# Optimization experiments

Hardware: AMD Instinct MI355X
Metric: run time of the kernel (lower is better)

## Reference

```python
import jax, jax.numpy as jnp
import numpy as np

B, S, K_IN = 8, 2048, 512
D_MODEL, N_INPUT, N_PROCESS = 1024, 4096, 2048
K = 256


def setup_inputs() -> dict:
    key = jax.random.key(0)
    k1, k2, k3, k4 = jax.random.split(key, 4)
    return {
        "selected_activations": jax.random.normal(k1, (B, S, K_IN), dtype=jnp.float32),
        "selected_indices": jax.random.randint(k2, (B, K_IN), 0, N_INPUT, dtype=jnp.int64),
        "k": K,
        "combination_weights": jax.random.normal(k3, (N_PROCESS, N_INPUT), dtype=jnp.float32),
        "output_projections": jax.random.normal(k4, (N_PROCESS, D_MODEL), dtype=jnp.float32),
    }


def reference(selected_activations, selected_indices, k, combination_weights, output_projections):
    # Gather per-batch combination weights: [n_process, B, k_in] -> [B, n_process, k_in]
    sel_w = jnp.take(combination_weights, selected_indices, axis=1)  # [P, B, k_in]
    sel_w = jnp.transpose(sel_w, (1, 0, 2))                          # [B, P, k_in]
    # Batched matmul + exact GELU (torch F.gelu default is erf-based)
    process_act = jax.nn.gelu(
        jnp.einsum("bsk,bpk->bsp", selected_activations, sel_w), approximate=False
    )  # [B, S, P]
    # Top-k gating over mean activation across sequence
    process_scores = process_act.mean(axis=1)                        # [B, P]
    _, proc_idx = jax.lax.top_k(process_scores, k)                   # [B, k]
    # Gather selected process activations along last dim
    sel_proc_act = jnp.take_along_axis(process_act, proc_idx[:, None, :], axis=2)  # [B, S, k]
    # Gather output projections per batch: [B, k, d_model]
    sel_proj = output_projections[proc_idx]                          # [B, k, D]
    return jnp.einsum("bsk,bkd->bsd", sel_proc_act, sel_proj)        # [B, S, D]
```

## Files before the change

### kernel.cpp

```cpp
#include <hip/hip_runtime.h>
#include <hip/hip_bf16.h>
#include <math.h>

#define B_    8
#define S_    2048
#define KIN_  512
#define NIN_  4096
#define P_    2048
#define D_    1024
#define KSEL_ 256

typedef __attribute__((ext_vector_type(8))) short short8;
typedef __attribute__((ext_vector_type(4))) float f32x4;

__device__ __forceinline__ unsigned short f2bf(float f) {
    unsigned u = __float_as_uint(f);
    unsigned r = (u + 0x7fffu + ((u >> 16) & 1u)) >> 16;
    return (unsigned short)r;
}
__device__ __forceinline__ float bf2f(unsigned short h) {
    return __uint_as_float(((unsigned)h) << 16);
}
__device__ __forceinline__ float gelu_exact(float x) {
    return 0.5f * x * (1.0f + erff(x * 0.70710678118654752f));
}
__device__ __forceinline__ void gl2lds16(const void* g, void* l) {
    __builtin_amdgcn_global_load_lds(
        (const __attribute__((address_space(1))) unsigned int*)g,
        (__attribute__((address_space(3))) unsigned int*)l, 16, 0, 0);
}

__global__ __launch_bounds__(256) void prep_kernel(
        const float* __restrict__ A, const float* __restrict__ W,
        const int* __restrict__ idx,
        unsigned short* __restrict__ Ahi, unsigned short* __restrict__ Alo,
        unsigned short* __restrict__ Ghi, unsigned short* __restrict__ Glo) {
    int id = blockIdx.x;
    if (id < 8192) {
        size_t i = (size_t)id * 256 + threadIdx.x;
        float4 v = reinterpret_cast<const float4*>(A)[i];
        ushort4 hi, lo;
        hi.x = f2bf(v.x); lo.x = f2bf(v.x - bf2f(hi.x));
        hi.y = f2bf(v.y); lo.y = f2bf(v.y - bf2f(hi.y));
        hi.z = f2bf(v.z); lo.z = f2bf(v.z - bf2f(hi.z));
        hi.w = f2bf(v.w); lo.w = f2bf(v.w - bf2f(hi.w));
        reinterpret_cast<ushort4*>(Ahi)[i] = hi;
        reinterpret_cast<ushort4*>(Alo)[i] = lo;
    } else {
        int bp = id - 8192;
        int b  = bp >> 11;
        const int* ib = idx + (size_t)b * KIN_;
        const float* wrow = W + (size_t)(bp & 2047) * NIN_;
        size_t o = (size_t)bp * KIN_;
        for (int j = threadIdx.x; j < KIN_; j += 256) {
            float v = wrow[ib[j]];
            unsigned short h = f2bf(v);
            Ghi[o + j] = h;
            Glo[o + j] = f2bf(v - bf2f(h));
        }
    }
}

template <bool STORE_C>
__global__ __launch_bounds__(256) void gemm1_score(
        const unsigned short* __restrict__ Ahi, const unsigned short* __restrict__ Alo,
        const unsigned short* __restrict__ Ghi, const unsigned short* __restrict__ Glo,
        float* __restrict__ scores, unsigned short* __restrict__ C) {
    __shared__ __align__(16) unsigned short lds[32768];

    int d    = blockIdx.x;
    int xcd  = d & 7;
    int slot = d >> 3;
    int c    = (slot >> 4) * 8 + xcd;
    int j    = slot & 15;
    int b    = c >> 4;
    int rc   = c & 15;
    int p0   = ((rc & 3) * 4 + (j & 3)) * 128;
    int s0   = ((rc >> 2) * 4 + (j >> 2)) * 128;

    const int t  = threadIdx.x;
    const int w = t >> 6, l = t & 63;
    const int wm = w & 1, wn = w >> 1;
    const int lr = l & 15, quad = l >> 4;

    const int srow = t >> 2;
    const int koff = (t & 3) * 8;
    const size_t baseA = ((size_t)(b * S_ + s0)) * KIN_;
    const size_t baseG = ((size_t)(b * P_ + p0)) * KIN_;
    const unsigned short* pA0 = Ahi + baseA + (size_t)srow * KIN_ + koff;
    const unsigned short* pA1 = pA0 + (size_t)64 * KIN_;
    const unsigned short* pL0 = Alo + baseA + (size_t)srow * KIN_ + koff;
    const unsigned short* pL1 = pL0 + (size_t)64 * KIN_;
    const unsigned short* pG0 = Ghi + baseG + (size_t)srow * KIN_ + koff;
    const unsigned short* pG1 = pG0 + (size_t)64 * KIN_;
    const unsigned short* pH0 = Glo + baseG + (size_t)srow * KIN_ + koff;
    const unsigned short* pH1 = pH0 + (size_t)64 * KIN_;
    char* lb = (char*)lds + w * 1024;

    int ra[4], rg[4];
#pragma unroll
    for (int i = 0; i < 4; i++) {
        ra[i] = (wm * 64 + i * 16 + lr) * 32 + quad * 8;
        rg[i] = (wn * 64 + i * 16 + lr) * 32 + quad * 8;
    }

    f32x4 acc[4][4];
#pragma unroll
    for (int i = 0; i < 4; i++)
#pragma unroll
        for (int jj = 0; jj < 4; jj++) acc[i][jj] = (f32x4){0.f, 0.f, 0.f, 0.f};

    auto issue = [&](int k0, int buf) {
        char* dst = lb + buf * 32768;
        gl2lds16(pA0 + k0, dst + 0);
        gl2lds16(pA1 + k0, dst + 4096);
        gl2lds16(pL0 + k0, dst + 8192);
        gl2lds16(pL1 + k0, dst + 12288);
        gl2lds16(pG0 + k0, dst + 16384);
        gl2lds16(pG1 + k0, dst + 20480);
        gl2lds16(pH0 + k0, dst + 24576);
        gl2lds16(pH1 + k0, dst + 28672);
    };

    issue(0, 0);
    for (int it = 0; it < KIN_ / 32; ++it) {
        if (it + 1 < KIN_ / 32) {
            issue((it + 1) * 32, (it + 1) & 1);
            asm volatile("s_waitcnt vmcnt(8)\n\ts_barrier" ::: "memory");
        } else {
            asm volatile("s_waitcnt vmcnt(0)\n\ts_barrier" ::: "memory");
        }
        const unsigned short* Lb = lds + (it & 1) * 16384;

        short8 gh[4], gl8[4];
#pragma unroll
        for (int i = 0; i < 4; i++) {
            gh[i]  = *(const short8*)(Lb + 8192 + rg[i]);
            gl8[i] = *(const short8*)(Lb + 12288 + rg[i]);
        }
#pragma unroll
        for (int mt = 0; mt < 4; mt++) {
            short8 ah = *(const short8*)(Lb + ra[mt]);
            short8 al = *(const short8*)(Lb + 4096 + ra[mt]);
#pragma unroll
            for (int nt = 0; nt < 4; nt++) {
                acc[mt][nt] = __builtin_amdgcn_mfma_f32_16x16x32_bf16(ah, gh[nt],  acc[mt][nt], 0, 0, 0);
                acc[mt][nt] = __builtin_amdgcn_mfma_f32_16x16x32_bf16(ah, gl8[nt], acc[mt][nt], 0, 0, 0);
                acc[mt][nt] = __builtin_amdgcn_mfma_f32_16x16x32_bf16(al, gh[nt],  acc[mt][nt], 0, 0, 0);
            }
        }
        asm volatile("s_barrier" ::: "memory");
    }

    float colsum[4] = {0.f, 0.f, 0.f, 0.f};
#pragma unroll
    for (int mt = 0; mt < 4; mt++)
#pragma unroll
        for (int nt = 0; nt < 4; nt++)
#pragma unroll
            for (int r = 0; r < 4; r++) {
                float g = gelu_exact(acc[mt][nt][r]);
                colsum[nt] += g;
                acc[mt][nt][r] = g;
            }
#pragma unroll
    for (int nt = 0; nt < 4; nt++) {
        colsum[nt] += __shfl_xor(colsum[nt], 16);
        colsum[nt] += __shfl_xor(colsum[nt], 32);
    }
    if (quad == 0) {
#pragma unroll
        for (int nt = 0; nt < 4; nt++)
            atomicAdd(&scores[b * P_ + p0 + wn * 64 + nt * 16 + lr], colsum[nt]);
    }

    if (STORE_C) {
#pragma unroll
        for (int mt = 0; mt < 4; mt++)
#pragma unroll
            for (int nt = 0; nt < 4; nt++)
#pragma unroll
                for (int r = 0; r < 4; r++) {
                    int row = wm * 64 + mt * 16 + quad * 4 + r;
                    int col = wn * 64 + nt * 16 + lr;
                    lds[row * 128 + col] = f2bf(acc[mt][nt][r]);
                }
        __syncthreads();
        for (int i = t; i < 2048; i += 256) {
            int row = i >> 4, ch = i & 15;
            uint4 v = *(const uint4*)(lds + row * 128 + ch * 8);
            *(uint4*)(C + ((size_t)(b * S_ + s0 + row)) * P_ + p0 + ch * 8) = v;
        }
    }
}

__global__ __launch_bounds__(1024) void topk_kernel(const float* __restrict__ scores,
                                                    int* __restrict__ pidx) {
    __shared__ float v[2048];
    __shared__ int   ix[2048];
    int b = blockIdx.x;
    int t = threadIdx.x;
    for (int i = t; i < 2048; i += 1024) { v[i] = scores[b * 2048 + i]; ix[i] = i; }
    __syncthreads();
    for (int k = 2; k <= 2048; k <<= 1) {
        for (int j = k >> 1; j > 0; j >>= 1) {
            for (int i = t; i < 2048; i += 1024) {
                int o = i ^ j;
                if (o > i) {
                    bool desc = ((i & k) == 0);
                    float va = v[i], vb = v[o];
                    int ia = ix[i], ib = ix[o];
                    bool b_first = (vb > va) || (vb == va && ib < ia);
                    if (desc == b_first) { v[i] = vb; v[o] = va; ix[i] = ib; ix[o] = ia; }
                }
            }
            __syncthreads();
        }
    }
    if (t < KSEL_) pidx[b * KSEL_ + t] = ix[t];
}

__global__ __launch_bounds__(256) void gathers_kernel(
        const unsigned short* __restrict__ C, const float* __restrict__ proj,
        const int* __restrict__ pidx,
        unsigned short* __restrict__ selact, unsigned short* __restrict__ PselT) {
    __shared__ int pj[256];
    __shared__ unsigned short tile[64][65];
    int id = blockIdx.x, t = threadIdx.x;
    if (id < 2048) {
        int b = id >> 8;
        pj[t] = pidx[b * KSEL_ + t];
        __syncthreads();
        size_t r0 = (size_t)b * S_ + (id & 255) * 8;
#pragma unroll
        for (int r = 0; r < 8; ++r) {
            size_t row = r0 + r;
            selact[row * KSEL_ + t] = C[row * P_ + pj[t]];
        }
    } else {
        int g = id - 2048;
        int d0 = (g & 15) * 64, k0 = ((g >> 4) & 3) * 64, b = g >> 6;
        int tr = t >> 6;
        int tc = t & 63;
#pragma unroll
        for (int r = 0; r < 16; r++) {
            int kk = r * 4 + tr;
            int prow = pidx[b * KSEL_ + k0 + kk];
            tile[kk][tc] = f2bf(proj[(size_t)prow * D_ + d0 + tc]);
        }
        __syncthreads();
#pragma unroll
        for (int r = 0; r < 16; r++) {
            int dd = r * 4 + tr;
            PselT[((size_t)(b * D_ + d0 + dd)) * KSEL_ + k0 + tc] = tile[tc][dd];
        }
    }
}

__global__ __launch_bounds__(256) void gemm1b_selact(
        const unsigned short* __restrict__ Ahi, const unsigned short* __restrict__ Alo,
        const unsigned short* __restrict__ Ghi, const unsigned short* __restrict__ Glo,
        const int* __restrict__ pidx, unsigned short* __restrict__ selact) {
    __shared__ __align__(16) unsigned short lds[16384];

    const int t  = threadIdx.x;
    const int b  = blockIdx.z;
    const int s0 = blockIdx.y * 128;
    const int n0 = blockIdx.x * 128;
    const int w = t >> 6, l = t & 63;
    const int wm = w & 1, wn = w >> 1;
    const int lr = l & 15, quad = l >> 4;

    const int srow = t >> 2;
    const int koff = (t & 3) * 8;
    const size_t baseA = ((size_t)(b * S_ + s0)) * KIN_;
    const size_t offA0 = baseA + (size_t)srow * KIN_ + koff;
    const size_t offA1 = offA0 + (size_t)64 * KIN_;
    const int prow0 = pidx[b * KSEL_ + n0 + srow];
    const int prow1 = pidx[b * KSEL_ + n0 + 64 + srow];
    const size_t offG0 = ((size_t)(b * P_ + prow0)) * KIN_ + koff;
    const size_t offG1 = ((size_t)(b * P_ + prow1)) * KIN_ + koff;
    char* lb = (char*)lds + w * 1024;

    int ra[4], rg[4];
#pragma unroll
    for (int i = 0; i < 4; i++) {
        ra[i] = (wm * 64 + i * 16 + lr) * 32 + quad * 8;
        rg[i] = (wn * 64 + i * 16 + lr) * 32 + quad * 8;
    }

    f32x4 acc[4][4];
#pragma unroll
    for (int i = 0; i < 4; i++)
#pragma unroll
        for (int j = 0; j < 4; j++) acc[i][j] = (f32x4){0.f, 0.f, 0.f, 0.f};

    for (int k0 = 0; k0 < KIN_; k0 += 32) {
        gl2lds16(Ahi + offA0 + k0, lb + 0);
        gl2lds16(Ahi + offA1 + k0, lb + 4096);
        gl2lds16(Alo + offA0 + k0, lb + 8192);
        gl2lds16(Alo + offA1 + k0, lb + 12288);
        gl2lds16(Ghi + offG0 + k0, lb + 16384);
        gl2lds16(Ghi + offG1 + k0, lb + 20480);
        gl2lds16(Glo + offG0 + k0, lb + 24576);
        gl2lds16(Glo + offG1 + k0, lb + 28672);
        __syncthreads();

        short8 ah[4], al8[4], gh[4], gl8[4];
#pragma unroll
        for (int i = 0; i < 4; i++) {
            ah[i]  = *(const short8*)(lds + ra[i]);
            al8[i] = *(const short8*)(lds + 4096 + ra[i]);
            gh[i]  = *(const short8*)(lds + 8192 + rg[i]);
            gl8[i] = *(const short8*)(lds + 12288 + rg[i]);
        }
#pragma unroll
        for (int mt = 0; mt < 4; mt++)
#pragma unroll
            for (int nt = 0; nt < 4; nt++) {
                acc[mt][nt] = __builtin_amdgcn_mfma_f32_16x16x32_bf16(ah[mt],  gh[nt],  acc[mt][nt], 0, 0, 0);
                acc[mt][nt] = __builtin_amdgcn_mfma_f32_16x16x32_bf16(ah[mt],  gl8[nt], acc[mt][nt], 0, 0, 0);
                acc[mt][nt] = __builtin_amdgcn_mfma_f32_16x16x32_bf16(al8[mt], gh[nt],  acc[mt][nt], 0, 0, 0);
            }
        __syncthreads();
    }

#pragma unroll
    for (int mt = 0; mt < 4; mt++)
#pragma unroll
        for (int nt = 0; nt < 4; nt++)
#pragma unroll
            for (int r = 0; r < 4; r++) {
                int row = wm * 64 + mt * 16 + quad * 4 + r;
                int col = wn * 64 + nt * 16 + lr;
                lds[row * 128 + col] = f2bf(gelu_exact(acc[mt][nt][r]));
            }
    __syncthreads();
    for (int i = t; i < 2048; i += 256) {
        int row = i >> 4, ch = i & 15;
        uint4 v = *(const uint4*)(lds + row * 128 + ch * 8);
        *(uint4*)(selact + ((size_t)(b * S_ + s0 + row)) * KSEL_ + n0 + ch * 8) = v;
    }
}

__global__ __launch_bounds__(256) void gemm2_mfma(
        const unsigned short* __restrict__ selact,
        const unsigned short* __restrict__ PselT,
        float* __restrict__ out) {
    __shared__ __align__(16) unsigned short lds[16384];

    const int t  = threadIdx.x;
    const int b  = blockIdx.z;
    const int s0 = blockIdx.y * 128;
    const int d0 = blockIdx.x * 128;
    const int w = t >> 6, l = t & 63;
    const int wm = w & 1, wn = w >> 1;
    const int lr = l & 15, quad = l >> 4;

    const int srow = t >> 2;
    const int koff = (t & 3) * 8;
    const unsigned short* pA0 = selact + ((size_t)(b * S_ + s0 + srow)) * KSEL_ + koff;
    const unsigned short* pA1 = pA0 + (size_t)64 * KSEL_;
    const unsigned short* pB0 = PselT + ((size_t)(b * D_ + d0 + srow)) * KSEL_ + koff;
    const unsigned short* pB1 = pB0 + (size_t)64 * KSEL_;
    char* lb = (char*)lds + w * 1024;

    int ra[4], rg[4];
#pragma unroll
    for (int i = 0; i < 4; i++) {
        ra[i] = (wm * 64 + i * 16 + lr) * 32 + quad * 8;
        rg[i] = (wn * 64 + i * 16 + lr) * 32 + quad * 8;
    }

    f32x4 acc[4][4];
#pragma unroll
    for (int i = 0; i < 4; i++)
#pragma unroll
        for (int j = 0; j < 4; j++) acc[i][j] = (f32x4){0.f, 0.f, 0.f, 0.f};

    auto issue = [&](int k0, int buf) {
        char* dst = lb + buf * 16384;
        gl2lds16(pA0 + k0, dst + 0);
        gl2lds16(pA1 + k0, dst + 4096);
        gl2lds16(pB0 + k0, dst + 8192);
        gl2lds16(pB1 + k0, dst + 12288);
    };

    issue(0, 0);
    for (int it = 0; it < KSEL_ / 32; ++it) {
        if (it + 1 < KSEL_ / 32) {
            issue((it + 1) * 32, (it + 1) & 1);
            asm volatile("s_waitcnt vmcnt(4)\n\ts_barrier" ::: "memory");
        } else {
            asm volatile("s_waitcnt vmcnt(0)\n\ts_barrier" ::: "memory");
        }
        const unsigned short* Lb = lds + (it & 1) * 8192;

        short8 af[4], bf[4];
#pragma unroll
        for (int i = 0; i < 4; i++) {
            af[i] = *(const short8*)(Lb + ra[i]);
            bf[i] = *(const short8*)(Lb + 4096 + rg[i]);
        }
#pragma unroll
        for (int mt = 0; mt < 4; mt++)
#pragma unroll
            for (int nt = 0; nt < 4; nt++)
                acc[mt][nt] = __builtin_amdgcn_mfma_f32_16x16x32_bf16(af[mt], bf[nt], acc[mt][nt], 0, 0, 0);
        asm volatile("s_barrier" ::: "memory");
    }

#pragma unroll
    for (int mt = 0; mt < 4; mt++)
#pragma unroll
        for (int nt = 0; nt < 4; nt++)
#pragma unroll
            for (int r = 0; r < 4; r++)
                out[((size_t)(b * S_ + s0 + wm * 64 + mt * 16 + quad * 4 + r)) * D_
                    + d0 + wn * 64 + nt * 16 + lr] = acc[mt][nt][r];
}

extern "C" void kernel_launch(void* const* d_in, const int* in_sizes, int n_in,
                              void* d_out, int out_size, void* d_ws, size_t ws_size,
                              hipStream_t stream) {
    (void)in_sizes; (void)n_in; (void)out_size;
    const float* act  = (const float*)d_in[0];
    const int*   idx  = (const int*)d_in[1];
    const float* W    = (const float*)d_in[3];
    const float* proj = (const float*)d_in[4];
    float*       out  = (float*)d_out;

    char* ws = (char*)d_ws;
    unsigned short* Ahi    = (unsigned short*)(ws + 0);
    unsigned short* Alo    = (unsigned short*)(ws + 16777216);
    unsigned short* Ghi    = (unsigned short*)(ws + 33554432);
    unsigned short* Glo    = (unsigned short*)(ws + 50331648);
    float*          scores = (float*)(ws + 67108864);
    int*            pidx   = (int*)(ws + 67174400);
    unsigned short* selact = (unsigned short*)(ws + 67182592);
    unsigned short* PselT  = (unsigned short*)(ws + 75571200);
    unsigned short* Cbf    = (unsigned short*)(ws + 79765504);
    const bool big = ws_size >= 146874368ull;

    hipMemsetAsync(scores, 0, B_ * P_ * sizeof(float), stream);

    prep_kernel<<<dim3(8192 + B_ * P_), 256, 0, stream>>>(act, W, idx, Ahi, Alo, Ghi, Glo);

    if (big) {
        gemm1_score<true><<<dim3(2048), 256, 0, stream>>>(Ahi, Alo, Ghi, Glo, scores, Cbf);
        topk_kernel<<<dim3(B_), 1024, 0, stream>>>(scores, pidx);
        gathers_kernel<<<dim3(2048 + 512), 256, 0, stream>>>(Cbf, proj, pidx, selact, PselT);
    } else {
        gemm1_score<false><<<dim3(2048), 256, 0, stream>>>(Ahi, Alo, Ghi, Glo, scores, nullptr);
        topk_kernel<<<dim3(B_), 1024, 0, stream>>>(scores, pidx);
        gemm1b_selact<<<dim3(KSEL_ / 128, S_ / 128, B_), 256, 0, stream>>>(
            Ahi, Alo, Ghi, Glo, pidx, selact);
        gathers_kernel<<<dim3(2048 + 512), 256, 0, stream>>>(Cbf, proj, pidx, selact, PselT);
    }
    gemm2_mfma<<<dim3(D_ / 128, S_ / 128, B_), 256, 0, stream>>>(selact, PselT, out);
}
```

Measured before the change: 403.3 us.

## Pre-swizzle A-lo into MFMA fragment layout, load directly to registers, XOR-swizzle LDS

The prep kernel now writes the low bf16 half of the activations in a fragment-major layout, so each lane can load its MFMA operand straight from global memory into registers. This removes the A-lo tiles from LDS staging, shrinking shared memory per block to allow three blocks per CU. LDS reads and writes in all GEMMs use an XOR swizzle on the k-chunk to reduce bank conflicts. The non-big path also stops launching the idle selact-gather blocks. The direct global loads add register pressure and rely on the cache for latency hiding.

```diff
diff --git a/kernel.cpp b/kernel.cpp
--- a/kernel.cpp
+++ b/kernel.cpp
@@ -36,23 +36,35 @@
         unsigned short* __restrict__ Ahi, unsigned short* __restrict__ Alo,
         unsigned short* __restrict__ Ghi, unsigned short* __restrict__ Glo) {
     int id = blockIdx.x;
-    if (id < 8192) {
-        size_t i = (size_t)id * 256 + threadIdx.x;
-        float4 v = reinterpret_cast<const float4*>(A)[i];
-        ushort4 hi, lo;
-        hi.x = f2bf(v.x); lo.x = f2bf(v.x - bf2f(hi.x));
-        hi.y = f2bf(v.y); lo.y = f2bf(v.y - bf2f(hi.y));
-        hi.z = f2bf(v.z); lo.z = f2bf(v.z - bf2f(hi.z));
-        hi.w = f2bf(v.w); lo.w = f2bf(v.w - bf2f(hi.w));
-        reinterpret_cast<ushort4*>(Ahi)[i] = hi;
-        reinterpret_cast<ushort4*>(Alo)[i] = lo;
+    int t  = threadIdx.x;
+    if (id < 1024) {
+        int b = id >> 7, rb = id & 127;
+        int l = t & 63, wv = t >> 6;
+        int lr = l & 15, quad = l >> 4;
+        const float* src = A + ((size_t)(b * S_ + rb * 16 + lr)) * KIN_ + quad * 8;
+        unsigned short* dh = Ahi + ((size_t)(b * S_ + rb * 16 + lr)) * KIN_ + quad * 8;
+        unsigned short* dl = Alo + (size_t)(b * 16) * 65536 + (size_t)rb * 512 + (size_t)l * 8;
+        for (int kb = wv; kb < 16; kb += 4) {
+            float4 v0 = *(const float4*)(src + kb * 32);
+            float4 v1 = *(const float4*)(src + kb * 32 + 4);
+            float vv[8] = {v0.x, v0.y, v0.z, v0.w, v1.x, v1.y, v1.z, v1.w};
+            short8 h8, l8;
+#pragma unroll
+            for (int jj = 0; jj < 8; jj++) {
+                unsigned short h = f2bf(vv[jj]);
+                h8[jj] = (short)h;
+                l8[jj] = (short)f2bf(vv[jj] - bf2f(h));
+            }
+            *(short8*)(dh + kb * 32) = h8;
+            *(short8*)(dl + (size_t)kb * 65536) = l8;
+        }
     } else {
-        int bp = id - 8192;
+        int bp = id - 1024;
         int b  = bp >> 11;
         const int* ib = idx + (size_t)b * KIN_;
         const float* wrow = W + (size_t)(bp & 2047) * NIN_;
         size_t o = (size_t)bp * KIN_;
-        for (int j = threadIdx.x; j < KIN_; j += 256) {
+        for (int j = t; j < KIN_; j += 256) {
             float v = wrow[ib[j]];
             unsigned short h = f2bf(v);
             Ghi[o + j] = h;
@@ -62,11 +74,11 @@
 }
 
 template <bool STORE_C>
-__global__ __launch_bounds__(256) void gemm1_score(
+__global__ __launch_bounds__(256, 3) void gemm1_score(
         const unsigned short* __restrict__ Ahi, const unsigned short* __restrict__ Alo,
         const unsigned short* __restrict__ Ghi, const unsigned short* __restrict__ Glo,
         float* __restrict__ scores, unsigned short* __restrict__ C) {
-    __shared__ __align__(16) unsigned short lds[32768];
+    __shared__ __align__(16) unsigned short lds[24576];
 
     int d    = blockIdx.x;
     int xcd  = d & 7;
@@ -84,24 +96,26 @@
     const int lr = l & 15, quad = l >> 4;
 
     const int srow = t >> 2;
-    const int koff = (t & 3) * 8;
+    const int koff = ((t & 3) ^ ((t >> 3) & 3)) * 8;
     const size_t baseA = ((size_t)(b * S_ + s0)) * KIN_;
     const size_t baseG = ((size_t)(b * P_ + p0)) * KIN_;
     const unsigned short* pA0 = Ahi + baseA + (size_t)srow * KIN_ + koff;
     const unsigned short* pA1 = pA0 + (size_t)64 * KIN_;
-    const unsigned short* pL0 = Alo + baseA + (size_t)srow * KIN_ + koff;
-    const unsigned short* pL1 = pL0 + (size_t)64 * KIN_;
     const unsigned short* pG0 = Ghi + baseG + (size_t)srow * KIN_ + koff;
     const unsigned short* pG1 = pG0 + (size_t)64 * KIN_;
     const unsigned short* pH0 = Glo + baseG + (size_t)srow * KIN_ + koff;
     const unsigned short* pH1 = pH0 + (size_t)64 * KIN_;
+    const unsigned short* alB = Alo + (size_t)(b * 16) * 65536
+                              + (size_t)((s0 >> 4) + wm * 4) * 512 + (size_t)l * 8;
     char* lb = (char*)lds + w * 1024;
 
     int ra[4], rg[4];
 #pragma unroll
     for (int i = 0; i < 4; i++) {
-        ra[i] = (wm * 64 + i * 16 + lr) * 32 + quad * 8;
-        rg[i] = (wn * 64 + i * 16 + lr) * 32 + quad * 8;
+        int rowa = wm * 64 + i * 16 + lr;
+        int rowg = wn * 64 + i * 16 + lr;
+        ra[i] = rowa * 32 + (quad ^ ((rowa >> 1) & 3)) * 8;
+        rg[i] = rowg * 32 + (quad ^ ((rowg >> 1) & 3)) * 8;
     }
 
     f32x4 acc[4][4];
@@ -111,42 +125,43 @@
         for (int jj = 0; jj < 4; jj++) acc[i][jj] = (f32x4){0.f, 0.f, 0.f, 0.f};
 
     auto issue = [&](int k0, int buf) {
-        char* dst = lb + buf * 32768;
+        char* dst = lb + buf * 24576;
         gl2lds16(pA0 + k0, dst + 0);
         gl2lds16(pA1 + k0, dst + 4096);
-        gl2lds16(pL0 + k0, dst + 8192);
-        gl2lds16(pL1 + k0, dst + 12288);
-        gl2lds16(pG0 + k0, dst + 16384);
-        gl2lds16(pG1 + k0, dst + 20480);
-        gl2lds16(pH0 + k0, dst + 24576);
-        gl2lds16(pH1 + k0, dst + 28672);
+        gl2lds16(pG0 + k0, dst + 8192);
+        gl2lds16(pG1 + k0, dst + 12288);
+        gl2lds16(pH0 + k0, dst + 16384);
+        gl2lds16(pH1 + k0, dst + 20480);
     };
 
     issue(0, 0);
     for (int it = 0; it < KIN_ / 32; ++it) {
+        short8 alc[4];
+#pragma unroll
+        for (int mt = 0; mt < 4; mt++)
+            alc[mt] = *(const short8*)(alB + (size_t)it * 65536 + mt * 512);
         if (it + 1 < KIN_ / 32) {
             issue((it + 1) * 32, (it + 1) & 1);
-            asm volatile("s_waitcnt vmcnt(8)\n\ts_barrier" ::: "memory");
+            asm volatile("s_waitcnt vmcnt(10)\n\ts_barrier" ::: "memory");
         } else {
             asm volatile("s_waitcnt vmcnt(0)\n\ts_barrier" ::: "memory");
         }
-        const unsigned short* Lb = lds + (it & 1) * 16384;
+        const unsigned short* Lb = lds + (it & 1) * 12288;
 
         short8 gh[4], gl8[4];
 #pragma unroll
         for (int i = 0; i < 4; i++) {
-            gh[i]  = *(const short8*)(Lb + 8192 + rg[i]);
-            gl8[i] = *(const short8*)(Lb + 12288 + rg[i]);
+            gh[i]  = *(const short8*)(Lb + 4096 + rg[i]);
+            gl8[i] = *(const short8*)(Lb + 8192 + rg[i]);
         }
 #pragma unroll
         for (int mt = 0; mt < 4; mt++) {
             short8 ah = *(const short8*)(Lb + ra[mt]);
-            short8 al = *(const short8*)(Lb + 4096 + ra[mt]);
 #pragma unroll
             for (int nt = 0; nt < 4; nt++) {
-                acc[mt][nt] = __builtin_amdgcn_mfma_f32_16x16x32_bf16(ah, gh[nt],  acc[mt][nt], 0, 0, 0);
-                acc[mt][nt] = __builtin_amdgcn_mfma_f32_16x16x32_bf16(ah, gl8[nt], acc[mt][nt], 0, 0, 0);
-                acc[mt][nt] = __builtin_amdgcn_mfma_f32_16x16x32_bf16(al, gh[nt],  acc[mt][nt], 0, 0, 0);
+                acc[mt][nt] = __builtin_amdgcn_mfma_f32_16x16x32_bf16(ah,      gh[nt],  acc[mt][nt], 0, 0, 0);
+                acc[mt][nt] = __builtin_amdgcn_mfma_f32_16x16x32_bf16(ah,      gl8[nt], acc[mt][nt], 0, 0, 0);
+                acc[mt][nt] = __builtin_amdgcn_mfma_f32_16x16x32_bf16(alc[mt], gh[nt],  acc[mt][nt], 0, 0, 0);
             }
         }
         asm volatile("s_barrier" ::: "memory");
@@ -223,10 +238,11 @@
 __global__ __launch_bounds__(256) void gathers_kernel(
         const unsigned short* __restrict__ C, const float* __restrict__ proj,
         const int* __restrict__ pidx,
-        unsigned short* __restrict__ selact, unsigned short* __restrict__ PselT) {
+        unsigned short* __restrict__ selact, unsigned short* __restrict__ PselT,
+        int base) {
     __shared__ int pj[256];
     __shared__ unsigned short tile[64][65];
-    int id = blockIdx.x, t = threadIdx.x;
+    int id = blockIdx.x + base, t = threadIdx.x;
     if (id < 2048) {
         int b = id >> 8;
         pj[t] = pidx[b * KSEL_ + t];
@@ -272,7 +288,7 @@
     const int lr = l & 15, quad = l >> 4;
 
     const int srow = t >> 2;
-    const int koff = (t & 3) * 8;
+    const int koff = ((t & 3) ^ ((t >> 3) & 3)) * 8;
     const size_t baseA = ((size_t)(b * S_ + s0)) * KIN_;
     const size_t offA0 = baseA + (size_t)srow * KIN_ + koff;
     const size_t offA1 = offA0 + (size_t)64 * KIN_;
@@ -280,48 +296,54 @@
     const int prow1 = pidx[b * KSEL_ + n0 + 64 + srow];
     const size_t offG0 = ((size_t)(b * P_ + prow0)) * KIN_ + koff;
     const size_t offG1 = ((size_t)(b * P_ + prow1)) * KIN_ + koff;
+    const unsigned short* alB = Alo + (size_t)(b * 16) * 65536
+                              + (size_t)((s0 >> 4) + wm * 4) * 512 + (size_t)l * 8;
     char* lb = (char*)lds + w * 1024;
 
     int ra[4], rg[4];
 #pragma unroll
     for (int i = 0; i < 4; i++) {
-        ra[i] = (wm * 64 + i * 16 + lr) * 32 + quad * 8;
-        rg[i] = (wn * 64 + i * 16 + lr) * 32 + quad * 8;
+        int rowa = wm * 64 + i * 16 + lr;
+        int rowg = wn * 64 + i * 16 + lr;
+        ra[i] = rowa * 32 + (quad ^ ((rowa >> 1) & 3)) * 8;
+        rg[i] = rowg * 32 + (quad ^ ((rowg >> 1) & 3)) * 8;
     }
 
     f32x4 acc[4][4];
 #pragma unroll
     for (int i = 0; i < 4; i++)
 #pragma unroll
-        for (int j = 0; j < 4; j++) acc[i][j] = (f32x4){0.f, 0.f, 0.f, 0.f};
+        for (int jj = 0; jj < 4; jj++) acc[i][jj] = (f32x4){0.f, 0.f, 0.f, 0.f};
 
     for (int k0 = 0; k0 < KIN_; k0 += 32) {
         gl2lds16(Ahi + offA0 + k0, lb + 0);
         gl2lds16(Ahi + offA1 + k0, lb + 4096);
-        gl2lds16(Alo + offA0 + k0, lb + 8192);
-        gl2lds16(Alo + offA1 + k0, lb + 12288);
-        gl2lds16(Ghi + offG0 + k0, lb + 16384);
-        gl2lds16(Ghi + offG1 + k0, lb + 20480);
-        gl2lds16(Glo + offG0 + k0, lb + 24576);
-        gl2lds16(Glo + offG1 + k0, lb + 28672);
+        gl2lds16(Ghi + offG0 + k0, lb + 8192);
+        gl2lds16(Ghi + offG1 + k0, lb + 12288);
+        gl2lds16(Glo + offG0 + k0, lb + 16384);
+        gl2lds16(Glo + offG1 + k0, lb + 20480);
+        short8 alc[4];
+#pragma unroll
+        for (int mt = 0; mt < 4; mt++)
+            alc[mt] = *(const short8*)(alB + (size_t)(k0 >> 5) * 65536 + mt * 512);
         __syncthreads();
 
-        short8 ah[4], al8[4], gh[4], gl8[4];
+        short8 gh[4], gl8[4];
 #pragma unroll
         for (int i = 0; i < 4; i++) {
-            ah[i]  = *(const short8*)(lds + ra[i]);
-            al8[i] = *(const short8*)(lds + 4096 + ra[i]);
-            gh[i]  = *(const short8*)(lds + 8192 + rg[i]);
-            gl8[i] = *(const short8*)(lds + 12288 + rg[i]);
-        }
-#pragma unroll
-        for (int mt = 0; mt < 4; mt++)
+            gh[i]  = *(const short8*)(lds + 4096 + rg[i]);
+            gl8[i] = *(const short8*)(lds + 8192 + rg[i]);
+        }
+#pragma unroll
+        for (int mt = 0; mt < 4; mt++) {
+            short8 ah = *(const short8*)(lds + ra[mt]);
 #pragma unroll
             for (int nt = 0; nt < 4; nt++) {
-                acc[mt][nt] = __builtin_amdgcn_mfma_f32_16x16x32_bf16(ah[mt],  gh[nt],  acc[mt][nt], 0, 0, 0);
-                acc[mt][nt] = __builtin_amdgcn_mfma_f32_16x16x32_bf16(ah[mt],  gl8[nt], acc[mt][nt], 0, 0, 0);
-                acc[mt][nt] = __builtin_amdgcn_mfma_f32_16x16x32_bf16(al8[mt], gh[nt],  acc[mt][nt], 0, 0, 0);
-            }
+                acc[mt][nt] = __builtin_amdgcn_mfma_f32_16x16x32_bf16(ah,      gh[nt],  acc[mt][nt], 0, 0, 0);
+                acc[mt][nt] = __builtin_amdgcn_mfma_f32_16x16x32_bf16(ah,      gl8[nt], acc[mt][nt], 0, 0, 0);
+                acc[mt][nt] = __builtin_amdgcn_mfma_f32_16x16x32_bf16(alc[mt], gh[nt],  acc[mt][nt], 0, 0, 0);
+            }
+        }
         __syncthreads();
     }
 
@@ -358,7 +380,7 @@
     const int lr = l & 15, quad = l >> 4;
 
     const int srow = t >> 2;
-    const int koff = (t & 3) * 8;
+    const int koff = ((t & 3) ^ ((t >> 3) & 3)) * 8;
     const unsigned short* pA0 = selact + ((size_t)(b * S_ + s0 + srow)) * KSEL_ + koff;
     const unsigned short* pA1 = pA0 + (size_t)64 * KSEL_;
     const unsigned short* pB0 = PselT + ((size_t)(b * D_ + d0 + srow)) * KSEL_ + koff;
@@ -368,15 +390,17 @@
     int ra[4], rg[4];
 #pragma unroll
     for (int i = 0; i < 4; i++) {
-        ra[i] = (wm * 64 + i * 16 + lr) * 32 + quad * 8;
-        rg[i] = (wn * 64 + i * 16 + lr) * 32 + quad * 8;
+        int rowa = wm * 64 + i * 16 + lr;
+        int rowg = wn * 64 + i * 16 + lr;
+        ra[i] = rowa * 32 + (quad ^ ((rowa >> 1) & 3)) * 8;
+        rg[i] = rowg * 32 + (quad ^ ((rowg >> 1) & 3)) * 8;
     }
 
     f32x4 acc[4][4];
 #pragma unroll
     for (int i = 0; i < 4; i++)
 #pragma unroll
-        for (int j = 0; j < 4; j++) acc[i][j] = (f32x4){0.f, 0.f, 0.f, 0.f};
+        for (int jj = 0; jj < 4; jj++) acc[i][jj] = (f32x4){0.f, 0.f, 0.f, 0.f};
 
     auto issue = [&](int k0, int buf) {
         char* dst = lb + buf * 16384;
@@ -444,18 +468,18 @@
 
     hipMemsetAsync(scores, 0, B_ * P_ * sizeof(float), stream);
 
-    prep_kernel<<<dim3(8192 + B_ * P_), 256, 0, stream>>>(act, W, idx, Ahi, Alo, Ghi, Glo);
+    prep_kernel<<<dim3(1024 + B_ * P_), 256, 0, stream>>>(act, W, idx, Ahi, Alo, Ghi, Glo);
 
     if (big) {
         gemm1_score<true><<<dim3(2048), 256, 0, stream>>>(Ahi, Alo, Ghi, Glo, scores, Cbf);
         topk_kernel<<<dim3(B_), 1024, 0, stream>>>(scores, pidx);
-        gathers_kernel<<<dim3(2048 + 512), 256, 0, stream>>>(Cbf, proj, pidx, selact, PselT);
+        gathers_kernel<<<dim3(2048 + 512), 256, 0, stream>>>(Cbf, proj, pidx, selact, PselT, 0);
     } else {
         gemm1_score<false><<<dim3(2048), 256, 0, stream>>>(Ahi, Alo, Ghi, Glo, scores, nullptr);
         topk_kernel<<<dim3(B_), 1024, 0, stream>>>(scores, pidx);
         gemm1b_selact<<<dim3(KSEL_ / 128, S_ / 128, B_), 256, 0, stream>>>(
             Ahi, Alo, Ghi, Glo, pidx, selact);
-        gathers_kernel<<<dim3(2048 + 512), 256, 0, stream>>>(Cbf, proj, pidx, selact, PselT);
+        gathers_kernel<<<dim3(512), 256, 0, stream>>>(Cbf, proj, pidx, selact, PselT, 2048);
     }
     gemm2_mfma<<<dim3(D_ / 128, S_ / 128, B_), 256, 0, stream>>>(selact, PselT, out);
 }
```

Result: faster. 364.0 us (-9.7%).
